# Performance work log

Hardware: AMD Instinct MI355X
Metric: run time of the kernel (lower is better)

Reference implementation:

```python
import jax, jax.numpy as jnp
import numpy as np

B, S, D = 16, 4096, 512
H, O = 2048, 512
E, TOP_K = 8, 2
CAP_FACTOR = 1.0
LN_EPS = 1e-5


def _capacity(num_tokens, num_experts, capacity_factor, multiple_of=4):
    c = int(round(num_tokens / num_experts * capacity_factor))
    c += -c % multiple_of
    return c


def setup_inputs() -> dict:
    key = jax.random.key(0)
    ks = jax.random.split(key, 8)
    T = B * S
    x = jax.random.normal(ks[0], (B, S, D), dtype=jnp.float32)
    noise = jax.random.normal(ks[1], (T, E), dtype=jnp.float32)
    # LayerNorm params
    gamma = jnp.ones((D,), jnp.float32)
    beta = jnp.zeros((D,), jnp.float32)
    # Router gate Linear(D, E)
    Wg = jax.random.normal(ks[2], (E, D), dtype=jnp.float32) / np.sqrt(D)
    bg = jnp.zeros((E,), jnp.float32)
    # Stacked expert FFN params: fc1 (D->H), fc2 (H->O)
    W1 = jax.random.normal(ks[3], (E, D, H), dtype=jnp.float32) / np.sqrt(D)
    b1 = jnp.zeros((E, H), jnp.float32)
    W2 = jax.random.normal(ks[4], (E, H, O), dtype=jnp.float32) / np.sqrt(H)
    b2 = jnp.zeros((E, O), jnp.float32)
    return {"x": x, "noise": noise, "gamma": gamma, "beta": beta,
            "Wg": Wg, "bg": bg, "W1": W1, "b1": b1, "W2": W2, "b2": b2}


def reference(x, noise, gamma, beta, Wg, bg, W1, b1, W2, b2):
    T = B * S
    xf = x.reshape(T, D)
    # LayerNorm
    mu = xf.mean(-1, keepdims=True)
    var = ((xf - mu) ** 2).mean(-1, keepdims=True)
    xn = (xf - mu) / jnp.sqrt(var + LN_EPS) * gamma + beta
    # Noisy token-choice router (eval mode -> aux_loss = 0)
    logits = xn @ Wg.T + bg                      # [T, E]
    noise_std = 1.0 / E
    gates_noisy = jax.nn.softmax(logits + noise_std * noise, axis=-1)
    topv, topi = jax.lax.top_k(gates_noisy, TOP_K)    # [T, K]
    topv = topv / (topv.sum(-1, keepdims=True) + 1e-20)
    flat_idx = topi.reshape(-1)                  # [T*K]
    flat_w = topv.reshape(-1)                    # [T*K]
    samp = jnp.repeat(jnp.arange(T), TOP_K)      # token id per routing slot
    capacity = _capacity(T, E, CAP_FACTOR)
    outputs = jnp.zeros((T, O), xf.dtype)
    processed = jnp.zeros((T,), bool)
    neg_inf = jnp.float32(-jnp.inf)
    for e in range(E):
        m = flat_idx == e
        w = jnp.where(m, flat_w, neg_inf)
        topw, pos = jax.lax.top_k(w, capacity)   # capacity-limited, by gate weight
        valid = jnp.isfinite(topw)
        tok = samp[pos]
        tok_safe = jnp.where(valid, tok, 0)
        xin = xn[tok_safe]                       # [capacity, D]
        h = jax.nn.gelu(xin @ W1[e] + b1[e], approximate=False)
        out = h @ W2[e] + b2[e]                  # [capacity, O]
        wv = jnp.where(valid, topw, 0.0)
        scat = jnp.where(valid, tok, T)          # out-of-range -> dropped
        outputs = outputs.at[scat].add(out * wv[:, None], mode='drop')
        processed = processed.at[scat].set(True, mode='drop')
    # Unprocessed (capacity-dropped or unrouted) tokens pass through normed x
    outputs = outputs + jnp.where(processed[:, None], 0.0, xn)
    aux_loss = jnp.zeros((), xf.dtype)
    return outputs.reshape(B, S, O), aux_loss
```

## Files before the change

kernel.cpp:

```cpp
#include <hip/hip_runtime.h>
#include <math.h>

typedef __attribute__((ext_vector_type(4))) float f32x4;
typedef __attribute__((ext_vector_type(8))) short short8;
typedef __attribute__((ext_vector_type(4))) short short4v;
typedef unsigned short u16;
typedef unsigned int u32;

#define T_TOKENS 65536
#define D_DIM    512
#define H_DIM    2048
#define O_DIM    512
#define E_NUM    8
#define CAP      8192

static constexpr size_t OFF_COUNTS = 0;
static constexpr size_t OFF_SELC   = 64;
static constexpr size_t OFF_BNDC   = 128;
static constexpr size_t OFF_PROC   = 192;
static constexpr size_t OFF_HIST   = OFF_PROC + (size_t)T_TOKENS * 4;
static constexpr size_t CTRL_BYTES = OFF_HIST + (size_t)E_NUM * 65536 * 4;
static constexpr size_t OFF_THR    = CTRL_BYTES;
static constexpr size_t OFF_REM    = OFF_THR + 64;
static constexpr size_t OFF_INV    = OFF_REM + 64;
static constexpr size_t OFF_CANDW  = OFF_INV + (size_t)T_TOKENS * 2 * 4;
static constexpr size_t OFF_CANDS  = OFF_CANDW + (size_t)E_NUM * T_TOKENS * 4;
static constexpr size_t OFF_SELTOK = OFF_CANDS + (size_t)E_NUM * T_TOKENS * 4;
static constexpr size_t OFF_SELW   = OFF_SELTOK + (size_t)E_NUM * CAP * 4;
static constexpr size_t OFF_LOG    = OFF_SELW + (size_t)E_NUM * CAP * 4;
static constexpr size_t OFF_BNDS   = OFF_LOG;
static constexpr size_t OFF_BNDW   = OFF_LOG + (size_t)E_NUM * CAP * 4 * 4;
static constexpr size_t OFF_XNB    = OFF_LOG + (size_t)T_TOKENS * E_NUM * 8;
static constexpr size_t OFF_W1T    = OFF_XNB + (size_t)T_TOKENS * D_DIM * 2;
static constexpr size_t OFF_W2T    = OFF_W1T + (size_t)E_NUM * D_DIM * H_DIM * 2;
static constexpr size_t OFF_H      = OFF_W2T + (size_t)E_NUM * H_DIM * O_DIM * 2;
static constexpr size_t OFF_FC2OUT = OFF_H + (size_t)E_NUM * CAP * H_DIM * 2;
static constexpr size_t NEED_BIG     = OFF_FC2OUT;
static constexpr size_t NEED_COMBINE = OFF_FC2OUT + (size_t)E_NUM * CAP * O_DIM * 2;

__device__ __forceinline__ u16 f2b(float f) {
    unsigned u = __float_as_uint(f);
    unsigned r = (u + 0x7FFFu + ((u >> 16) & 1u)) >> 16;
    return (u16)r;
}
__device__ __forceinline__ float b2f(u16 b) {
    return __uint_as_float(((unsigned)b) << 16);
}
__device__ __forceinline__ u32 f2b_pack(float lo, float hi) {
    return (u32)f2b(lo) | ((u32)f2b(hi) << 16);
}

__device__ __forceinline__ float gelu_fast(float x) {
    float x2 = x * x;
    float arg = x * fmaf(0.0713548162726f, x2, 1.59576912161f);
    float t = __expf(arg);
    float r = __builtin_amdgcn_rcpf(t + 1.0f);
    return x * (1.0f - r);
}

#define AS1 __attribute__((address_space(1)))
#define AS3 __attribute__((address_space(3)))

__global__ __launch_bounds__(256) void ln_kernel(
    const float* __restrict__ x, const float* __restrict__ gamma,
    const float* __restrict__ beta, const float* __restrict__ Wg,
    u16* __restrict__ xnb, double* __restrict__ logits)
{
    __shared__ float sWg[E_NUM * D_DIM];
    for (int i = threadIdx.x; i < E_NUM * D_DIM; i += 256) sWg[i] = Wg[i];
    __syncthreads();

    const int wave = threadIdx.x >> 6, lane = threadIdx.x & 63;

    for (int it = 0; it < 16; ++it) {
        const int t = blockIdx.x * 64 + it * 4 + wave;
        const float2* xr2 = (const float2*)(x + (size_t)t * D_DIM);

        float2 xv[4];
        #pragma unroll
        for (int i = 0; i < 4; i++) xv[i] = xr2[i * 64 + lane];

        double s = 0.0;
        #pragma unroll
        for (int i = 0; i < 4; i++) s += (double)xv[i].x + (double)xv[i].y;
        #pragma unroll
        for (int o = 32; o > 0; o >>= 1) s += __shfl_xor(s, o);
        double mu = s / 512.0;

        double v = 0.0;
        #pragma unroll
        for (int i = 0; i < 4; i++) {
            double d0 = (double)xv[i].x - mu, d1 = (double)xv[i].y - mu;
            v += d0 * d0 + d1 * d1;
        }
        #pragma unroll
        for (int o = 32; o > 0; o >>= 1) v += __shfl_xor(v, o);
        double rstd = 1.0 / sqrt(v / 512.0 + 1e-5);

        float xnf[8];
        u32* xno = (u32*)(xnb + (size_t)t * D_DIM);
        #pragma unroll
        for (int i = 0; i < 4; i++) {
            int c = i * 128 + lane * 2;
            float2 g2 = ((const float2*)gamma)[i * 64 + lane];
            float2 b2v = ((const float2*)beta)[i * 64 + lane];
            double xd0 = ((double)xv[i].x - mu) * rstd * (double)g2.x + (double)b2v.x;
            double xd1 = ((double)xv[i].y - mu) * rstd * (double)g2.y + (double)b2v.y;
            xnf[2 * i]     = (float)xd0;
            xnf[2 * i + 1] = (float)xd1;
            xno[i * 64 + lane] = f2b_pack(xnf[2 * i], xnf[2 * i + 1]);
            (void)c;
        }

        double p[E_NUM];
        #pragma unroll
        for (int e = 0; e < E_NUM; e++) p[e] = 0.0;
        #pragma unroll
        for (int i = 0; i < 4; i++) {
            int c = i * 128 + lane * 2;
            double xd0 = (double)xnf[2 * i];
            double xd1 = (double)xnf[2 * i + 1];
            #pragma unroll
            for (int e = 0; e < E_NUM; e++)
                p[e] += xd0 * (double)sWg[e * D_DIM + c] + xd1 * (double)sWg[e * D_DIM + c + 1];
        }
        #pragma unroll
        for (int o = 32; o > 0; o >>= 1) {
            #pragma unroll
            for (int e = 0; e < E_NUM; e++) p[e] += __shfl_xor(p[e], o);
        }
        if (lane < 8) {
            double vv = p[0];
            #pragma unroll
            for (int e = 1; e < 8; e++) if (lane == e) vv = p[e];
            logits[(size_t)t * 8 + lane] = vv;
        }
    }
}

__global__ __launch_bounds__(256) void gate_kernel(
    const double* __restrict__ logits, const float* __restrict__ noise,
    const float* __restrict__ bg,
    int* __restrict__ counts, float* __restrict__ cand_w, int* __restrict__ cand_slot,
    unsigned int* __restrict__ hist)
{
    __shared__ int lcnt[E_NUM], lbase[E_NUM];
    if (threadIdx.x < E_NUM) lcnt[threadIdx.x] = 0;
    __syncthreads();
    const int t = blockIdx.x * 256 + threadIdx.x;

    double l[E_NUM], m = -1e300;
    #pragma unroll
    for (int e = 0; e < E_NUM; e++) {
        l[e] = logits[(size_t)t * 8 + e] + (double)bg[e] + 0.125 * (double)noise[(size_t)t * 8 + e];
        if (l[e] > m) m = l[e];
    }
    double sum = 0.0, g[E_NUM];
    #pragma unroll
    for (int e = 0; e < E_NUM; e++) { g[e] = exp(l[e] - m); sum += g[e]; }
    double inv = 1.0 / sum;
    #pragma unroll
    for (int e = 0; e < E_NUM; e++) g[e] *= inv;

    double v1 = -1.0; int i1 = 0;
    #pragma unroll
    for (int e = 0; e < E_NUM; e++) if (g[e] > v1) { v1 = g[e]; i1 = e; }
    double v2 = -1.0; int i2 = 0;
    #pragma unroll
    for (int e = 0; e < E_NUM; e++) if (e != i1 && g[e] > v2) { v2 = g[e]; i2 = e; }

    double denom = v1 + v2 + 1e-20;
    float w1 = (float)(v1 / denom);
    float w2 = (float)(v2 / denom);

    atomicAdd(&hist[(size_t)i1 * 65536 + ((~__float_as_uint(w1)) >> 16)], 1u);
    atomicAdd(&hist[(size_t)i2 * 65536 + ((~__float_as_uint(w2)) >> 16)], 1u);

    int p1 = atomicAdd(&lcnt[i1], 1);
    int p2 = atomicAdd(&lcnt[i2], 1);
    __syncthreads();
    if (threadIdx.x < E_NUM) lbase[threadIdx.x] = atomicAdd(&counts[threadIdx.x], lcnt[threadIdx.x]);
    __syncthreads();
    cand_w[(size_t)i1 * T_TOKENS + lbase[i1] + p1] = w1;
    cand_slot[(size_t)i1 * T_TOKENS + lbase[i1] + p1] = 2 * t;
    cand_w[(size_t)i2 * T_TOKENS + lbase[i2] + p2] = w2;
    cand_slot[(size_t)i2 * T_TOKENS + lbase[i2] + p2] = 2 * t + 1;
}

__global__ __launch_bounds__(1024) void scan_kernel(
    const unsigned int* __restrict__ hist, const int* __restrict__ counts,
    int* __restrict__ thr16, int* __restrict__ rem)
{
    const int e = blockIdx.x;
    const int n = counts[e];
    if (n <= CAP) {
        if (threadIdx.x == 0) { thr16[e] = 65536; rem[e] = 0; }
        return;
    }
    const unsigned int* h = hist + (size_t)e * 65536;
    __shared__ unsigned int part[1024];
    const int tid = threadIdx.x;
    unsigned int own = 0;
    const int base = tid * 64;
    #pragma unroll 8
    for (int i = 0; i < 64; i++) own += h[base + i];
    part[tid] = own;
    __syncthreads();
    for (int off = 1; off < 1024; off <<= 1) {
        unsigned int v = (tid >= off) ? part[tid - off] : 0u;
        __syncthreads();
        part[tid] += v;
        __syncthreads();
    }
    unsigned int incl = part[tid];
    unsigned int excl = incl - own;
    const unsigned int need = CAP;
    if (excl < need && incl >= need) {
        unsigned int cum = excl;
        for (int i = 0; i < 64; i++) {
            unsigned int hv = h[base + i];
            if (cum + hv >= need) { thr16[e] = base + i; rem[e] = (int)(need - cum); break; }
            cum += hv;
        }
    }
}

__global__ __launch_bounds__(256) void emit_kernel(
    const int* __restrict__ counts, const float* __restrict__ cand_w,
    const int* __restrict__ cand_slot, const int* __restrict__ thr16,
    int* __restrict__ sel_count, int* __restrict__ sel_tok, float* __restrict__ sel_w,
    int* __restrict__ bnd_count, int* __restrict__ bnd_slot, float* __restrict__ bnd_w,
    int* __restrict__ processed, u32* __restrict__ inv)
{
    const int e = blockIdx.y;
    const int n = counts[e];
    const int thr = thr16[e];
    const float* cw = cand_w + (size_t)e * T_TOKENS;
    const int* cs = cand_slot + (size_t)e * T_TOKENS;
    for (int i = blockIdx.x * 256 + threadIdx.x; i < n; i += gridDim.x * 256) {
        float w = cw[i];
        int slot = cs[i];
        int p16 = (int)((~__float_as_uint(w)) >> 16);
        if (p16 < thr) {
            int pos = atomicAdd(&sel_count[e], 1);
            sel_tok[e * CAP + pos] = slot >> 1;
            sel_w[e * CAP + pos]  = w;
            processed[slot >> 1] = 1;
            inv[slot] = ((u32)e << 16) | (u32)pos;
        } else if (p16 == thr) {
            int bpos = atomicAdd(&bnd_count[e], 1);
            bnd_slot[(size_t)e * CAP * 4 + bpos] = slot;
            bnd_w[(size_t)e * CAP * 4 + bpos]   = w;
        }
    }
}

__global__ __launch_bounds__(256) void boundary_kernel(
    const int* __restrict__ bnd_count, const int* __restrict__ bnd_slot,
    const float* __restrict__ bnd_w, const int* __restrict__ rem,
    int* __restrict__ sel_count, int* __restrict__ sel_tok, float* __restrict__ sel_w,
    int* __restrict__ processed, u32* __restrict__ inv)
{
    const int e = blockIdx.x;
    const int r = rem[e];
    if (r == 0) return;
    const int nb = bnd_count[e];
    const int* bs = bnd_slot + (size_t)e * CAP * 4;
    const float* bw = bnd_w + (size_t)e * CAP * 4;
    for (int i = threadIdx.x; i < nb; i += 256) {
        unsigned long long ki = (((unsigned long long)(~__float_as_uint(bw[i]))) << 32) | (unsigned int)bs[i];
        int rank = 0;
        for (int j = 0; j < nb; j++) {
            unsigned long long kj = (((unsigned long long)(~__float_as_uint(bw[j]))) << 32) | (unsigned int)bs[j];
            rank += (kj < ki);
        }
        if (rank < r) {
            int pos = atomicAdd(&sel_count[e], 1);
            sel_tok[e * CAP + pos] = bs[i] >> 1;
            sel_w[e * CAP + pos]  = bw[i];
            processed[bs[i] >> 1] = 1;
            inv[bs[i]] = ((u32)e << 16) | (u32)pos;
        }
    }
}

__global__ __launch_bounds__(256) void convert_wt_kernel(
    const float* __restrict__ W, u16* __restrict__ Wt, int K, int N)
{
    __shared__ float tile[64][65];
    const int e = blockIdx.z;
    const int k0 = blockIdx.y * 64, n0 = blockIdx.x * 64;
    const float* We = W + (size_t)e * K * N;
    u16* Wte = Wt + (size_t)e * N * K;
    const int tx = threadIdx.x & 63, ty = threadIdx.x >> 6;
    #pragma unroll
    for (int r = 0; r < 64; r += 4)
        tile[ty + r][tx] = We[(size_t)(k0 + ty + r) * N + n0 + tx];
    __syncthreads();
    #pragma unroll
    for (int r = 0; r < 64; r += 4) {
        int nn = ty + r;
        Wte[(size_t)(n0 + nn) * K + k0 + tx] = f2b(tile[tx][nn]);
    }
}

__global__ __launch_bounds__(256) void init_out_kernel(
    const u16* __restrict__ xnb, const int* __restrict__ processed, float* __restrict__ out)
{
    size_t i = (size_t)blockIdx.x * 256 + threadIdx.x;
    int t = (int)(i >> 7);
    float4 v; v.x = 0.f; v.y = 0.f; v.z = 0.f; v.w = 0.f;
    if (!processed[t]) {
        const u16* xp = xnb + (i << 2);
        v.x = b2f(xp[0]); v.y = b2f(xp[1]); v.z = b2f(xp[2]); v.w = b2f(xp[3]);
    }
    ((float4*)out)[i] = v;
}

__global__ __launch_bounds__(256) void combine_kernel(
    const u16* __restrict__ fc2out, const u32* __restrict__ inv,
    const u16* __restrict__ xnb, float* __restrict__ out)
{
    size_t i = (size_t)blockIdx.x * 256 + threadIdx.x;
    int t = (int)(i >> 7);
    int c4 = (int)(i & 127);
    u32 a = inv[2 * t], b = inv[2 * t + 1];
    float4 v; v.x = 0.f; v.y = 0.f; v.z = 0.f; v.w = 0.f;
    bool any = false;
    if (a != 0xFFFFFFFFu) {
        const u16* p = fc2out + ((size_t)(a >> 16) * CAP + (a & 0xFFFFu)) * O_DIM + c4 * 4;
        short4v pv = *(const short4v*)p;
        v.x += b2f((u16)pv.x); v.y += b2f((u16)pv.y); v.z += b2f((u16)pv.z); v.w += b2f((u16)pv.w);
        any = true;
    }
    if (b != 0xFFFFFFFFu) {
        const u16* p = fc2out + ((size_t)(b >> 16) * CAP + (b & 0xFFFFu)) * O_DIM + c4 * 4;
        short4v pv = *(const short4v*)p;
        v.x += b2f((u16)pv.x); v.y += b2f((u16)pv.y); v.z += b2f((u16)pv.z); v.w += b2f((u16)pv.w);
        any = true;
    }
    if (!any) {
        const u16* xp = xnb + (i << 2);
        v.x = b2f(xp[0]); v.y = b2f(xp[1]); v.z = b2f(xp[2]); v.w = b2f(xp[3]);
    }
    ((float4*)out)[i] = v;
}

template<int GATHER, int EPI, int MERGED, int KT>
__global__ __launch_bounds__(256, 4) void moe_gemm_kernel(
    const u16* __restrict__ Abase, const u16* __restrict__ Btbase,
    const float* __restrict__ biasbase,
    const int* __restrict__ sel_tok, const float* __restrict__ sel_w,
    const int* __restrict__ sel_count, int e_arg, int N,
    size_t a_estride, size_t h_estride,
    u16* __restrict__ h_out, u16* __restrict__ out16, float* __restrict__ outf)
{
    __shared__ u16 sA[128 * 64];
    __shared__ u16 sB[128 * 64];

    const int e = MERGED ? blockIdx.z : e_arg;
    const int selc = sel_count[e];
    const int row0 = blockIdx.x * 128;
    if (row0 >= selc) return;
    const int n0 = blockIdx.y * 128;

    const u16* A = Abase + (size_t)e * a_estride;
    const u16* Bt = Btbase + (size_t)e * (size_t)N * KT;
    const float* bias = biasbase + (size_t)e * N;
    const int* sel_tok_e = sel_tok + (size_t)e * CAP;
    const float* sel_w_e = sel_w + (size_t)e * CAP;

    const int t = threadIdx.x;
    const int lane = t & 63;
    const int w = t >> 6;
    const int wm = (w >> 1) * 64;
    const int wn = (w & 1) * 64;
    const int lr = lane & 15;
    const int lg = lane >> 4;

    const int srow = t >> 3;
    const int sk   = (((t & 7) ^ (srow & 7)) * 8);

    u32 aoff[4];
    #pragma unroll
    for (int i = 0; i < 4; i++) {
        int r = row0 + i * 32 + srow;
        int gr;
        if (GATHER) gr = (r < selc) ? sel_tok_e[r] : 0;
        else        gr = r;
        aoff[i] = (u32)gr * (u32)KT + (u32)sk;
    }
    u32 boff[4];
    #pragma unroll
    for (int i = 0; i < 4; i++) {
        int nn = n0 + i * 32 + srow;
        boff[i] = (u32)nn * (u32)KT + (u32)sk;
    }

    f32x4 acc[4][4] = {};

    for (int kt = 0; kt < KT / 64; ++kt) {
        const int ko = kt << 6;
        #pragma unroll
        for (int i = 0; i < 4; i++)
            __builtin_amdgcn_global_load_lds((const AS1 void*)(A + aoff[i] + ko),
                                             (AS3 void*)&sA[i * 2048 + t * 8], 16, 0, 0);
        #pragma unroll
        for (int i = 0; i < 4; i++)
            __builtin_amdgcn_global_load_lds((const AS1 void*)(Bt + boff[i] + ko),
                                             (AS3 void*)&sB[i * 2048 + t * 8], 16, 0, 0);
        asm volatile("s_waitcnt vmcnt(0)" ::: "memory");
        __builtin_amdgcn_s_barrier();

        __builtin_amdgcn_s_setprio(1);
        #pragma unroll
        for (int kk = 0; kk < 64; kk += 32) {
            short8 bf[4];
            #pragma unroll
            for (int n = 0; n < 4; n++) {
                int br = wn + n * 16 + lr;
                bf[n] = *(const short8*)&sB[br * 64 + ((kk + lg * 8) ^ ((br & 7) * 8))];
            }
            #pragma unroll
            for (int m = 0; m < 4; m++) {
                int ar = wm + m * 16 + lr;
                short8 af = *(const short8*)&sA[ar * 64 + ((kk + lg * 8) ^ ((ar & 7) * 8))];
                #pragma unroll
                for (int n = 0; n < 4; n++)
                    acc[m][n] = __builtin_amdgcn_mfma_f32_16x16x32_bf16(af, bf[n], acc[m][n], 0, 0, 0);
            }
        }
        __builtin_amdgcn_s_setprio(0);
        __builtin_amdgcn_s_barrier();
    }

    if (EPI == 0) {
        u16* hO = h_out + (size_t)e * h_estride;
        #pragma unroll
        for (int m = 0; m < 4; m++) {
            int row = row0 + wm + m * 16 + lg * 4;
            #pragma unroll
            for (int n = 0; n < 4; n++) {
                int col = n0 + wn + n * 16 + lr;
                float bb = bias[col];
                #pragma unroll
                for (int r = 0; r < 4; r++) {
                    float vv = acc[m][n][r] + bb;
                    hO[(size_t)(row + r) * N + col] = f2b(gelu_fast(vv));
                }
            }
        }
    } else if (EPI == 3) {
        #pragma unroll
        for (int m = 0; m < 4; m++) {
            int row = row0 + wm + m * 16 + lg * 4;
            #pragma unroll
            for (int r = 0; r < 4; r++) {
                int rr = row + r;
                if (rr < selc) {
                    float wgt = sel_w_e[rr];
                    u16* orow = out16 + ((size_t)e * CAP + rr) * O_DIM;
                    #pragma unroll
                    for (int n = 0; n < 4; n++) {
                        int col = n0 + wn + n * 16 + lr;
                        orow[col] = f2b(wgt * (acc[m][n][r] + bias[col]));
                    }
                }
            }
        }
    } else {
        #pragma unroll
        for (int m = 0; m < 4; m++) {
            int row = row0 + wm + m * 16 + lg * 4;
            #pragma unroll
            for (int r = 0; r < 4; r++) {
                int rr = row + r;
                if (rr < selc) {
                    int tok = sel_tok_e[rr];
                    float wgt = sel_w_e[rr];
                    float* orow = outf + (size_t)tok * O_DIM;
                    #pragma unroll
                    for (int n = 0; n < 4; n++) {
                        int col = n0 + wn + n * 16 + lr;
                        atomicAdd(&orow[col], wgt * (acc[m][n][r] + bias[col]));
                    }
                }
            }
        }
    }
}

extern "C" void kernel_launch(void* const* d_in, const int* in_sizes, int n_in,
                              void* d_out, int out_size, void* d_ws, size_t ws_size,
                              hipStream_t stream) {
    const float* x     = (const float*)d_in[0];
    const float* noise = (const float*)d_in[1];
    const float* gamma = (const float*)d_in[2];
    const float* beta  = (const float*)d_in[3];
    const float* Wg    = (const float*)d_in[4];
    const float* bg    = (const float*)d_in[5];
    const float* W1    = (const float*)d_in[6];
    const float* b1    = (const float*)d_in[7];
    const float* W2    = (const float*)d_in[8];
    const float* b2    = (const float*)d_in[9];
    float* out = (float*)d_out;

    char* ws = (char*)d_ws;
    int*    counts    = (int*)(ws + OFF_COUNTS);
    int*    sel_count = (int*)(ws + OFF_SELC);
    int*    bnd_count = (int*)(ws + OFF_BNDC);
    int*    processed = (int*)(ws + OFF_PROC);
    unsigned int* hist = (unsigned int*)(ws + OFF_HIST);
    int*    thr16     = (int*)(ws + OFF_THR);
    int*    rem       = (int*)(ws + OFF_REM);
    u32*    inv       = (u32*)(ws + OFF_INV);
    float*  cand_w    = (float*)(ws + OFF_CANDW);
    int*    cand_slot = (int*)(ws + OFF_CANDS);
    int*    sel_tok   = (int*)(ws + OFF_SELTOK);
    float*  sel_w     = (float*)(ws + OFF_SELW);
    double* logits    = (double*)(ws + OFF_LOG);
    int*    bnd_slot  = (int*)(ws + OFF_BNDS);
    float*  bnd_w     = (float*)(ws + OFF_BNDW);
    u16*    xnb       = (u16*)(ws + OFF_XNB);
    u16*    W1t       = (u16*)(ws + OFF_W1T);
    u16*    W2t       = (u16*)(ws + OFF_W2T);
    u16*    h         = (u16*)(ws + OFF_H);
    u16*    fc2out    = (u16*)(ws + OFF_FC2OUT);

    const bool use_combine = (ws_size >= NEED_COMBINE);

    hipMemsetAsync(ws, 0, CTRL_BYTES, stream);
    if (use_combine)
        hipMemsetAsync(ws + OFF_INV, 0xFF, (size_t)T_TOKENS * 2 * 4, stream);
    hipMemsetAsync((char*)d_out + (size_t)T_TOKENS * O_DIM * 4, 0, 4, stream);

    convert_wt_kernel<<<dim3(H_DIM / 64, D_DIM / 64, E_NUM), 256, 0, stream>>>(W1, W1t, D_DIM, H_DIM);
    convert_wt_kernel<<<dim3(O_DIM / 64, H_DIM / 64, E_NUM), 256, 0, stream>>>(W2, W2t, H_DIM, O_DIM);

    ln_kernel<<<T_TOKENS / 64, 256, 0, stream>>>(x, gamma, beta, Wg, xnb, logits);
    gate_kernel<<<T_TOKENS / 256, 256, 0, stream>>>(logits, noise, bg, counts, cand_w, cand_slot, hist);
    scan_kernel<<<E_NUM, 1024, 0, stream>>>(hist, counts, thr16, rem);
    emit_kernel<<<dim3(64, E_NUM), 256, 0, stream>>>(counts, cand_w, cand_slot, thr16,
                                                     sel_count, sel_tok, sel_w,
                                                     bnd_count, bnd_slot, bnd_w, processed, inv);
    boundary_kernel<<<E_NUM, 256, 0, stream>>>(bnd_count, bnd_slot, bnd_w, rem,
                                               sel_count, sel_tok, sel_w, processed, inv);

    if (use_combine) {
        moe_gemm_kernel<1, 0, 1, D_DIM><<<dim3(CAP / 128, H_DIM / 128, E_NUM), 256, 0, stream>>>(
            xnb, W1t, b1, sel_tok, sel_w, sel_count, 0, H_DIM,
            0, (size_t)CAP * H_DIM, h, nullptr, nullptr);
        moe_gemm_kernel<0, 3, 1, H_DIM><<<dim3(CAP / 128, O_DIM / 128, E_NUM), 256, 0, stream>>>(
            h, W2t, b2, sel_tok, sel_w, sel_count, 0, O_DIM,
            (size_t)CAP * H_DIM, 0, nullptr, fc2out, nullptr);
        combine_kernel<<<(T_TOKENS * O_DIM / 4) / 256, 256, 0, stream>>>(fc2out, inv, xnb, out);
    } else if (ws_size >= NEED_BIG) {
        init_out_kernel<<<(T_TOKENS * O_DIM / 4) / 256, 256, 0, stream>>>(xnb, processed, out);
        moe_gemm_kernel<1, 0, 1, D_DIM><<<dim3(CAP / 128, H_DIM / 128, E_NUM), 256, 0, stream>>>(
            xnb, W1t, b1, sel_tok, sel_w, sel_count, 0, H_DIM,
            0, (size_t)CAP * H_DIM, h, nullptr, nullptr);
        moe_gemm_kernel<0, 2, 1, H_DIM><<<dim3(CAP / 128, O_DIM / 128, E_NUM), 256, 0, stream>>>(
            h, W2t, b2, sel_tok, sel_w, sel_count, 0, O_DIM,
            (size_t)CAP * H_DIM, 0, nullptr, nullptr, out);
    } else {
        init_out_kernel<<<(T_TOKENS * O_DIM / 4) / 256, 256, 0, stream>>>(xnb, processed, out);
        for (int e = 0; e < E_NUM; e++) {
            moe_gemm_kernel<1, 0, 0, D_DIM><<<dim3(CAP / 128, H_DIM / 128), 256, 0, stream>>>(
                xnb, W1t, b1, sel_tok, sel_w, sel_count, e, H_DIM,
                0, 0, h, nullptr, nullptr);
            moe_gemm_kernel<0, 2, 0, H_DIM><<<dim3(CAP / 128, O_DIM / 128), 256, 0, stream>>>(
                h, W2t, b2, sel_tok, sel_w, sel_count, e, O_DIM,
                0, 0, nullptr, nullptr, out);
        }
    }
}
```

Before: 707.5 us.

## Double-buffer GEMM K-tiles in LDS with async prefetch of next tile

```diff
diff --git a/kernel.cpp b/kernel.cpp
--- a/kernel.cpp
+++ b/kernel.cpp
@@ -101,7 +101,6 @@
         u32* xno = (u32*)(xnb + (size_t)t * D_DIM);
         #pragma unroll
         for (int i = 0; i < 4; i++) {
-            int c = i * 128 + lane * 2;
             float2 g2 = ((const float2*)gamma)[i * 64 + lane];
             float2 b2v = ((const float2*)beta)[i * 64 + lane];
             double xd0 = ((double)xv[i].x - mu) * rstd * (double)g2.x + (double)b2v.x;
@@ -109,7 +108,6 @@
             xnf[2 * i]     = (float)xd0;
             xnf[2 * i + 1] = (float)xd1;
             xno[i * 64 + lane] = f2b_pack(xnf[2 * i], xnf[2 * i + 1]);
-            (void)c;
         }
 
         double p[E_NUM];
@@ -355,8 +353,8 @@
     size_t a_estride, size_t h_estride,
     u16* __restrict__ h_out, u16* __restrict__ out16, float* __restrict__ outf)
 {
-    __shared__ u16 sA[128 * 64];
-    __shared__ u16 sB[128 * 64];
+    __shared__ u16 sA[2 * 128 * 32];
+    __shared__ u16 sB[2 * 128 * 32];
 
     const int e = MERGED ? blockIdx.z : e_arg;
     const int selc = sel_count[e];
@@ -378,53 +376,70 @@
     const int lr = lane & 15;
     const int lg = lane >> 4;
 
-    const int srow = t >> 3;
-    const int sk   = (((t & 7) ^ (srow & 7)) * 8);
-
-    u32 aoff[4];
-    #pragma unroll
-    for (int i = 0; i < 4; i++) {
-        int r = row0 + i * 32 + srow;
+    const int srow_lo = t >> 2;
+    const u32 swz = (u32)(((t & 3) ^ ((t >> 3) & 3)) * 8);
+
+    u32 aoff[2];
+    #pragma unroll
+    for (int i = 0; i < 2; i++) {
+        int r = row0 + i * 64 + srow_lo;
         int gr;
         if (GATHER) gr = (r < selc) ? sel_tok_e[r] : 0;
         else        gr = r;
-        aoff[i] = (u32)gr * (u32)KT + (u32)sk;
-    }
-    u32 boff[4];
-    #pragma unroll
-    for (int i = 0; i < 4; i++) {
-        int nn = n0 + i * 32 + srow;
-        boff[i] = (u32)nn * (u32)KT + (u32)sk;
+        aoff[i] = (u32)gr * (u32)KT + swz;
+    }
+    u32 boff[2];
+    #pragma unroll
+    for (int i = 0; i < 2; i++) {
+        int nn = n0 + i * 64 + srow_lo;
+        boff[i] = (u32)nn * (u32)KT + swz;
     }
 
     f32x4 acc[4][4] = {};
-
-    for (int kt = 0; kt < KT / 64; ++kt) {
-        const int ko = kt << 6;
-        #pragma unroll
-        for (int i = 0; i < 4; i++)
-            __builtin_amdgcn_global_load_lds((const AS1 void*)(A + aoff[i] + ko),
-                                             (AS3 void*)&sA[i * 2048 + t * 8], 16, 0, 0);
-        #pragma unroll
-        for (int i = 0; i < 4; i++)
-            __builtin_amdgcn_global_load_lds((const AS1 void*)(Bt + boff[i] + ko),
-                                             (AS3 void*)&sB[i * 2048 + t * 8], 16, 0, 0);
-        asm volatile("s_waitcnt vmcnt(0)" ::: "memory");
+    constexpr int NH = KT / 32;
+
+    #pragma unroll
+    for (int i = 0; i < 2; i++)
+        __builtin_amdgcn_global_load_lds((const AS1 void*)(A + aoff[i]),
+                                         (AS3 void*)&sA[0 * 4096 + i * 2048 + t * 8], 16, 0, 0);
+    #pragma unroll
+    for (int i = 0; i < 2; i++)
+        __builtin_amdgcn_global_load_lds((const AS1 void*)(Bt + boff[i]),
+                                         (AS3 void*)&sB[0 * 4096 + i * 2048 + t * 8], 16, 0, 0);
+
+    for (int kh = 0; kh < NH; ++kh) {
+        const int cur = kh & 1;
+        if (kh + 1 < NH) {
+            const int nxt = cur ^ 1;
+            const int ko = (kh + 1) * 32;
+            #pragma unroll
+            for (int i = 0; i < 2; i++)
+                __builtin_amdgcn_global_load_lds((const AS1 void*)(A + aoff[i] + ko),
+                                                 (AS3 void*)&sA[nxt * 4096 + i * 2048 + t * 8], 16, 0, 0);
+            #pragma unroll
+            for (int i = 0; i < 2; i++)
+                __builtin_amdgcn_global_load_lds((const AS1 void*)(Bt + boff[i] + ko),
+                                                 (AS3 void*)&sB[nxt * 4096 + i * 2048 + t * 8], 16, 0, 0);
+            asm volatile("s_waitcnt vmcnt(4)" ::: "memory");
+        } else {
+            asm volatile("s_waitcnt vmcnt(0)" ::: "memory");
+        }
         __builtin_amdgcn_s_barrier();
 
+        const u16* sAc = &sA[cur * 4096];
+        const u16* sBc = &sB[cur * 4096];
         __builtin_amdgcn_s_setprio(1);
-        #pragma unroll
-        for (int kk = 0; kk < 64; kk += 32) {
+        {
             short8 bf[4];
             #pragma unroll
             for (int n = 0; n < 4; n++) {
                 int br = wn + n * 16 + lr;
-                bf[n] = *(const short8*)&sB[br * 64 + ((kk + lg * 8) ^ ((br & 7) * 8))];
+                bf[n] = *(const short8*)&sBc[br * 32 + ((lg ^ ((br >> 1) & 3)) * 8)];
             }
             #pragma unroll
             for (int m = 0; m < 4; m++) {
                 int ar = wm + m * 16 + lr;
-                short8 af = *(const short8*)&sA[ar * 64 + ((kk + lg * 8) ^ ((ar & 7) * 8))];
+                short8 af = *(const short8*)&sAc[ar * 32 + ((lg ^ ((ar >> 1) & 3)) * 8)];
                 #pragma unroll
                 for (int n = 0; n < 4; n++)
                     acc[m][n] = __builtin_amdgcn_mfma_f32_16x16x32_bf16(af, bf[n], acc[m][n], 0, 0, 0);
```

After: 668.5 us. 5.5% less time.
